# Optimization experiments

Hardware: AMD Instinct MI355X
Metric: run time of the kernel (lower is better)

Reference implementation:

```python
import jax, jax.numpy as jnp
import numpy as np

B, T, D, H = 4096, 256, 64, 96
NEG_SLOPE = 0.01


def setup_inputs() -> dict:
    key = jax.random.key(0)
    ks = jax.random.split(key, 13)
    def n(k, shape, s=0.1):
        return jax.random.normal(k, shape, jnp.float32) * s
    return {
        "x": jax.random.normal(ks[0], (B, T, D), jnp.float32),
        # layer 0 LSTM (PyTorch gate order i,f,g,o); b = b_ih + b_hh fused
        "Wih0": n(ks[1], (4 * H, D)), "Whh0": n(ks[2], (4 * H, H)), "b0": n(ks[3], (4 * H,)),
        # layer 1 LSTM
        "Wih1": n(ks[4], (4 * H, H)), "Whh1": n(ks[5], (4 * H, H)), "b1": n(ks[6], (4 * H,)),
        # MLP head
        "fcW1": n(ks[7], (H, H)), "fcb1": n(ks[8], (H,)),
        "fcW2": n(ks[9], (H, H)), "fcb2": n(ks[10], (H,)),
        "fcW3": n(ks[11], (1, H)), "fcb3": n(ks[12], (1,)),
    }


def _cell(x_t, h, c, Wih, Whh, b):
    # gates: [B, 4H], PyTorch order i, f, g, o
    g = x_t @ Wih.T + h @ Whh.T + b
    i, f, gg, o = jnp.split(g, 4, axis=-1)
    i = jax.nn.sigmoid(i)
    f = jax.nn.sigmoid(f)
    gg = jnp.tanh(gg)
    o = jax.nn.sigmoid(o)
    c_new = f * c + i * gg
    h_new = o * jnp.tanh(c_new)
    return h_new, c_new


def reference(x, Wih0, Whh0, b0, Wih1, Whh1, b1, fcW1, fcb1, fcW2, fcb2, fcW3, fcb3):
    Bx = x.shape[0]
    Hx = Whh0.shape[1]
    xT = jnp.swapaxes(x, 0, 1)  # [T, B, D]
    init = tuple(jnp.zeros((Bx, Hx), x.dtype) for _ in range(4))

    def step(carry, xt):
        h1, c1, h2, c2 = carry
        h1, c1 = _cell(xt, h1, c1, Wih0, Whh0, b0)
        h2, c2 = _cell(h1, h2, c2, Wih1, Whh1, b1)
        return (h1, c1, h2, c2), None

    (h1, c1, h2, c2), _ = jax.lax.scan(step, init, xT)
    last = h2  # out[:, -1, :] == final hidden state of layer 2
    z = jax.nn.leaky_relu(last @ fcW1.T + fcb1, NEG_SLOPE)
    z = jax.nn.leaky_relu(z @ fcW2.T + fcb2, NEG_SLOPE)
    return (z @ fcW3.T + fcb3).squeeze(-1)  # [B]
```

## Files before the change

### kernel.cpp

```cpp
#include <hip/hip_runtime.h>
#include <hip/hip_bf16.h>

#define TT 256
#define NB 16
#define NTHR 768

typedef float f32x4 __attribute__((ext_vector_type(4)));
typedef _Float16 f16x8 __attribute__((ext_vector_type(8)));
typedef __fp16 fp16x2 __attribute__((ext_vector_type(2)));

#define XPAN  0
#define H1PAN 4096
#define H2PAN 12288
#define H2F32 20480
#define FCZ   26624
#define LDSZ  38912

__device__ __forceinline__ float vexp2(float x) { float r; asm("v_exp_f32 %0, %1" : "=v"(r) : "v"(x)); return r; }
__device__ __forceinline__ float vrcp(float x)  { float r; asm("v_rcp_f32 %0, %1" : "=v"(r) : "v"(x)); return r; }
#define L2E 1.44269504f

#define MFMA16(a, b, c) __builtin_amdgcn_mfma_f32_16x16x32_f16(a, b, c, 0, 0, 0)

__device__ __forceinline__ unsigned short f2h_bits(float f) {
    union { _Float16 h; unsigned short u; } cv; cv.h = (_Float16)f; return cv.u;
}

union PK8 { f16x8 v8; fp16x2 v2[4]; };
__device__ __forceinline__ f16x8 pack8(const f32x4& a, const f32x4& b) {
    PK8 U;
    U.v2[0] = __builtin_amdgcn_cvt_pkrtz(a[0], a[1]);
    U.v2[1] = __builtin_amdgcn_cvt_pkrtz(a[2], a[3]);
    U.v2[2] = __builtin_amdgcn_cvt_pkrtz(b[0], b[1]);
    U.v2[3] = __builtin_amdgcn_cvt_pkrtz(b[2], b[3]);
    return U.v8;
}

__global__ void prep_frags16(const float* __restrict__ Wih0, const float* __restrict__ Whh0,
                             const float* __restrict__ Wih1, const float* __restrict__ Whh1,
                             unsigned short* __restrict__ wsf2) {
    int s = blockIdx.x;
    int e = threadIdx.x;
    int i = e & 7, col = (e >> 3) & 15, kg = e >> 7;
    float wv;
    if (s < 48) {
        int ks = s / 24, nt = s % 24;
        int k = ks * 32 + kg * 8 + i, cg = nt * 16 + col;
        wv = Wih0[cg * 64 + k];
    } else if (s < 120) {
        int j = (s - 48) / 24, nt = (s - 48) % 24;
        int k = j * 32 + kg * 8 + i, cg = nt * 16 + col;
        wv = Whh0[cg * 96 + k];
    } else {
        int s2 = s - 120;
        int j = s2 / 24, nt = s2 % 24;
        int k = j * 32 + kg * 8 + i, cg = nt * 16 + col;
        wv = (k < 96) ? Wih1[cg * 96 + k] : Whh1[cg * 96 + (k - 96)];
    }
    wsf2[s * 512 + e] = f2h_bits(wv);
}

__global__ __launch_bounds__(NTHR, 3) void lstm_main(
    const float* __restrict__ x,
    const float* __restrict__ b0, const float* __restrict__ b1,
    const float* __restrict__ fcW1, const float* __restrict__ fcb1,
    const float* __restrict__ fcW2, const float* __restrict__ fcb2,
    const float* __restrict__ fcW3, const float* __restrict__ fcb3,
    const unsigned short* __restrict__ wsf2,
    float* __restrict__ out)
{
    __shared__ __align__(16) char LDS[LDSZ];

    const int tid = threadIdx.x;
    const int lane = tid & 63;
    const int w = tid >> 6;
    const int isB = (w ^ (w >> 2)) & 1;
    const int ub = w >> 1;
    const int l15 = lane & 15, kg = lane >> 4, r7 = l15 & 7;
    const int blk = blockIdx.x;
    const float* xblk = x + (size_t)blk * NB * TT * 64;

    #pragma unroll 1
    for (int i = tid; i < 4096; i += NTHR) ((int*)(LDS + H1PAN))[i] = 0;

    const int cb = ub * 2 + (l15 >> 3);
    const int lo2 = (l15 & 7) * 2;

    const bool stg = (w < 4) && (lane < 32);
    const int st = w * 32 + lane;
    const int sr = st >> 3, su = st & 7;
    const float* xsrc = xblk + (size_t)sr * TT * 64 + su * 8;
    const int xoff = sr * 128 + ((su ^ (sr & 7)) << 4);
    f32x4 xa, xb;

    if (stg) {
        xa = *(const f32x4*)xsrc; xb = *(const f32x4*)(xsrc + 4);
        *(f16x8*)(LDS + XPAN + xoff) = pack8(xa, xb);
    }

    if (!isB) {
        f16x8 F0x[4][2], F0h[4][3];
        #pragma unroll
        for (int g = 0; g < 4; ++g) {
            #pragma unroll
            for (int ks = 0; ks < 2; ++ks)
                F0x[g][ks] = *(const f16x8*)(wsf2 + (ks * 24 + g * 6 + ub) * 512 + lane * 8);
            #pragma unroll
            for (int j = 0; j < 3; ++j)
                F0h[g][j] = *(const f16x8*)(wsf2 + (48 + j * 24 + g * 6 + ub) * 512 + lane * 8);
        }
        float bias[4];
        #pragma unroll
        for (int g = 0; g < 4; ++g) bias[g] = b0[g * 96 + ub * 16 + l15];

        f32x4 c1 = {0.f, 0.f, 0.f, 0.f};
        __syncthreads();

        #pragma unroll 1
        for (int s = 0; s <= TT; ++s) {
            if (stg && s + 1 < TT) {
                const float* xp = xsrc + (size_t)(s + 1) * 64;
                xa = *(const f32x4*)xp; xb = *(const f32x4*)(xp + 4);
            }
            if (s < TT) {
                const char* xr  = LDS + XPAN + ((s & 1) << 11);
                const char* h1r = LDS + H1PAN + (((s & 1) ^ 1) << 12);
                f32x4 a[4];
                #pragma unroll
                for (int g = 0; g < 4; ++g) a[g] = (f32x4){bias[g], bias[g], bias[g], bias[g]};
                __builtin_amdgcn_s_setprio(1);
                #pragma unroll
                for (int ks = 0; ks < 2; ++ks) {
                    int off = l15 * 128 + (((ks * 4 + kg) ^ r7) << 4);
                    f16x8 xh = *(const f16x8*)(xr + off);
                    #pragma unroll
                    for (int g = 0; g < 4; ++g) a[g] = MFMA16(xh, F0x[g][ks], a[g]);
                }
                #pragma unroll
                for (int j = 0; j < 3; ++j) {
                    int off = l15 * 256 + (((j * 4 + kg) ^ r7) << 4);
                    f16x8 ah = *(const f16x8*)(h1r + off);
                    #pragma unroll
                    for (int g = 0; g < 4; ++g) a[g] = MFMA16(ah, F0h[g][j], a[g]);
                }
                __builtin_amdgcn_s_setprio(0);
                char* h1w = LDS + H1PAN + ((s & 1) << 12);
                #pragma unroll
                for (int q = 0; q < 4; ++q) {
                    float ei = vexp2(a[0][q] * (-L2E));
                    float ef = vexp2(a[1][q] * (-L2E));
                    float eg = vexp2(a[2][q] * (-2.f * L2E));
                    float eo = vexp2(a[3][q] * (-L2E));
                    float ivgv = (1.f - eg) * vrcp((1.f + ei) * (1.f + eg));
                    float fv = vrcp(1.f + ef);
                    float cn = fmaf(fv, c1[q], ivgv);
                    c1[q] = cn;
                    float ec = vexp2(cn * (-2.f * L2E));
                    float h = (1.f - ec) * vrcp((1.f + eo) * (1.f + ec));
                    int r_ = kg * 4 + q;
                    int off = r_ * 256 + ((cb ^ (r_ & 7)) << 4) + lo2;
                    *(unsigned short*)(h1w + off) = f2h_bits(h);
                }
            }
            if (stg && s + 1 < TT)
                *(f16x8*)(LDS + XPAN + (((s + 1) & 1) << 11) + xoff) = pack8(xa, xb);
            __syncthreads();
        }
    } else {
        f16x8 F1[4][6];
        #pragma unroll
        for (int g = 0; g < 4; ++g)
            #pragma unroll
            for (int j = 0; j < 6; ++j)
                F1[g][j] = *(const f16x8*)(wsf2 + (120 + j * 24 + g * 6 + ub) * 512 + lane * 8);
        float bias[4];
        #pragma unroll
        for (int g = 0; g < 4; ++g) bias[g] = b1[g * 96 + ub * 16 + l15];

        f32x4 c2 = {0.f, 0.f, 0.f, 0.f};
        __syncthreads();

        #pragma unroll 1
        for (int s = 0; s <= TT; ++s) {
            if (stg && s + 1 < TT) {
                const float* xp = xsrc + (size_t)(s + 1) * 64;
                xa = *(const f32x4*)xp; xb = *(const f32x4*)(xp + 4);
            }
            if (s >= 1) {
                const char* h1r = LDS + H1PAN + (((s & 1) ^ 1) << 12);
                const char* h2r = LDS + H2PAN + ((s & 1) << 12);
                f32x4 a[4];
                #pragma unroll
                for (int g = 0; g < 4; ++g) a[g] = (f32x4){bias[g], bias[g], bias[g], bias[g]};
                __builtin_amdgcn_s_setprio(1);
                #pragma unroll
                for (int j = 0; j < 6; ++j) {
                    const char* pan = (j < 3) ? h1r : h2r;
                    int cc = (j < 3) ? j : j - 3;
                    int off = l15 * 256 + (((cc * 4 + kg) ^ r7) << 4);
                    f16x8 ah = *(const f16x8*)(pan + off);
                    #pragma unroll
                    for (int g = 0; g < 4; ++g) a[g] = MFMA16(ah, F1[g][j], a[g]);
                }
                __builtin_amdgcn_s_setprio(0);
                char* h2w = LDS + H2PAN + ((~s & 1) << 12);
                #pragma unroll
                for (int q = 0; q < 4; ++q) {
                    float ei = vexp2(a[0][q] * (-L2E));
                    float ef = vexp2(a[1][q] * (-L2E));
                    float eg = vexp2(a[2][q] * (-2.f * L2E));
                    float eo = vexp2(a[3][q] * (-L2E));
                    float ivgv = (1.f - eg) * vrcp((1.f + ei) * (1.f + eg));
                    float fv = vrcp(1.f + ef);
                    float cn = fmaf(fv, c2[q], ivgv);
                    c2[q] = cn;
                    float ec = vexp2(cn * (-2.f * L2E));
                    float h = (1.f - ec) * vrcp((1.f + eo) * (1.f + ec));
                    int r_ = kg * 4 + q;
                    int off = r_ * 256 + ((cb ^ (r_ & 7)) << 4) + lo2;
                    *(unsigned short*)(h2w + off) = f2h_bits(h);
                    if (s == TT)
                        ((float*)(LDS + H2F32))[(ub * 16 + l15) * 16 + r_] = h;
                }
            }
            if (stg && s + 1 < TT)
                *(f16x8*)(LDS + XPAN + (((s + 1) & 1) << 11) + xoff) = pack8(xa, xb);
            __syncthreads();
        }
    }
    __syncthreads();

    const float* h2f = (const float*)(LDS + H2F32);
    float* z1 = (float*)(LDS + FCZ);
    float* z2 = z1 + 1536;
    if (tid < 192) {
        int u = tid % 96, half = tid / 96;
        float s0 = fcb1[u];
        for (int r = half * 8; r < half * 8 + 8; ++r) {
            float s = s0;
            #pragma unroll 4
            for (int k = 0; k < 96; ++k) s += fcW1[u * 96 + k] * h2f[k * 16 + r];
            z1[r * 96 + u] = s > 0.f ? s : 0.01f * s;
        }
    }
    __syncthreads();
    if (tid < 192) {
        int u = tid % 96, half = tid / 96;
        float s0 = fcb2[u];
        for (int r = half * 8; r < half * 8 + 8; ++r) {
            float s = s0;
            #pragma unroll 4
            for (int k = 0; k < 96; ++k) s += fcW2[u * 96 + k] * z1[r * 96 + k];
            z2[r * 96 + u] = s > 0.f ? s : 0.01f * s;
        }
    }
    __syncthreads();
    if (tid < NB) {
        float s = fcb3[0];
        #pragma unroll 4
        for (int k = 0; k < 96; ++k) s += fcW3[k] * z2[tid * 96 + k];
        out[blk * NB + tid] = s;
    }
}

extern "C" void kernel_launch(void* const* d_in, const int* in_sizes, int n_in,
                              void* d_out, int out_size, void* d_ws, size_t ws_size,
                              hipStream_t stream) {
    const float* x    = (const float*)d_in[0];
    const float* Wih0 = (const float*)d_in[1];
    const float* Whh0 = (const float*)d_in[2];
    const float* b0   = (const float*)d_in[3];
    const float* Wih1 = (const float*)d_in[4];
    const float* Whh1 = (const float*)d_in[5];
    const float* b1   = (const float*)d_in[6];
    const float* fcW1 = (const float*)d_in[7];
    const float* fcb1 = (const float*)d_in[8];
    const float* fcW2 = (const float*)d_in[9];
    const float* fcb2 = (const float*)d_in[10];
    const float* fcW3 = (const float*)d_in[11];
    const float* fcb3 = (const float*)d_in[12];

    unsigned short* wsf2 = (unsigned short*)d_ws;

    prep_frags16<<<264, 512, 0, stream>>>(Wih0, Whh0, Wih1, Whh1, wsf2);
    lstm_main<<<256, NTHR, 0, stream>>>(x, b0, b1, fcW1, fcb1, fcW2, fcb2,
                                        fcW3, fcb3, wsf2, (float*)d_out);
}
```

Baseline: 406.5 us.

## Replace per-step block barriers with LDS counter-based producer/consumer pipeline

Drops the per-timestep __syncthreads shared by both LSTM layers. Layer-0 and layer-1 wave groups now coordinate through workgroup-scope atomic counters in LDS, using 4-deep ring buffers for the h1 and h2 panels, so the two layers can drift up to a few steps apart. X staging moves onto layer-0 waves only, and the loop drops the extra skew iteration. The aim is to remove lockstep barrier stalls and let layer 0 run ahead, at the cost of spin-wait polling with s_sleep, more LDS, and subtler memory-ordering correctness.

```diff
diff --git a/kernel.cpp b/kernel.cpp
--- a/kernel.cpp
+++ b/kernel.cpp
@@ -11,10 +11,11 @@
 
 #define XPAN  0
 #define H1PAN 4096
-#define H2PAN 12288
-#define H2F32 20480
-#define FCZ   26624
-#define LDSZ  38912
+#define H2PAN 20480
+#define H2F32 36864
+#define FCZ   43008
+#define CNT   55296
+#define LDSZ  55360
 
 __device__ __forceinline__ float vexp2(float x) { float r; asm("v_exp_f32 %0, %1" : "=v"(r) : "v"(x)); return r; }
 __device__ __forceinline__ float vrcp(float x)  { float r; asm("v_rcp_f32 %0, %1" : "=v"(r) : "v"(x)); return r; }
@@ -34,6 +35,19 @@
     U.v2[2] = __builtin_amdgcn_cvt_pkrtz(b[0], b[1]);
     U.v2[3] = __builtin_amdgcn_cvt_pkrtz(b[2], b[3]);
     return U.v8;
+}
+
+__device__ __forceinline__ void spinge(int* cnt, int target) {
+    if (target > 0) {
+        while (__hip_atomic_load(cnt, __ATOMIC_RELAXED, __HIP_MEMORY_SCOPE_WORKGROUP) < target)
+            __builtin_amdgcn_s_sleep(1);
+        __threadfence_block();
+    }
+}
+__device__ __forceinline__ void signal(int* cnt, int lane) {
+    __threadfence_block();
+    if (lane == 0)
+        __hip_atomic_fetch_add(cnt, 1, __ATOMIC_RELAXED, __HIP_MEMORY_SCOPE_WORKGROUP);
 }
 
 __global__ void prep_frags16(const float* __restrict__ Wih0, const float* __restrict__ Whh0,
@@ -80,14 +94,20 @@
     const int blk = blockIdx.x;
     const float* xblk = x + (size_t)blk * NB * TT * 64;
 
+    int* prodH1 = (int*)(LDS + CNT);
+    int* consH1 = (int*)(LDS + CNT) + 1;
+    int* prodH2 = (int*)(LDS + CNT) + 2;
+
     #pragma unroll 1
-    for (int i = tid; i < 4096; i += NTHR) ((int*)(LDS + H1PAN))[i] = 0;
+    for (int i = tid; i < 8192; i += NTHR) ((int*)(LDS + H1PAN))[i] = 0;
+    if (tid < 16) ((int*)(LDS + CNT))[tid] = 0;
 
     const int cb = ub * 2 + (l15 >> 3);
     const int lo2 = (l15 & 7) * 2;
 
-    const bool stg = (w < 4) && (lane < 32);
-    const int st = w * 32 + lane;
+    const int sidx = (w == 0) ? 0 : (w == 2) ? 1 : (w == 5) ? 2 : 3;
+    const bool stg = (w == 0 || w == 2 || w == 5 || w == 7) && (lane < 32);
+    const int st = sidx * 32 + lane;
     const int sr = st >> 3, su = st & 7;
     const float* xsrc = xblk + (size_t)sr * TT * 64 + su * 8;
     const int xoff = sr * 128 + ((su ^ (sr & 7)) << 4);
@@ -97,6 +117,7 @@
         xa = *(const f32x4*)xsrc; xb = *(const f32x4*)(xsrc + 4);
         *(f16x8*)(LDS + XPAN + xoff) = pack8(xa, xb);
     }
+    __syncthreads();
 
     if (!isB) {
         f16x8 F0x[4][2], F0h[4][3];
@@ -114,57 +135,56 @@
         for (int g = 0; g < 4; ++g) bias[g] = b0[g * 96 + ub * 16 + l15];
 
         f32x4 c1 = {0.f, 0.f, 0.f, 0.f};
-        __syncthreads();
 
         #pragma unroll 1
-        for (int s = 0; s <= TT; ++s) {
+        for (int s = 0; s < TT; ++s) {
             if (stg && s + 1 < TT) {
                 const float* xp = xsrc + (size_t)(s + 1) * 64;
                 xa = *(const f32x4*)xp; xb = *(const f32x4*)(xp + 4);
             }
-            if (s < TT) {
-                const char* xr  = LDS + XPAN + ((s & 1) << 11);
-                const char* h1r = LDS + H1PAN + (((s & 1) ^ 1) << 12);
-                f32x4 a[4];
+            spinge(prodH1, 6 * s);
+            const char* xr  = LDS + XPAN + ((s & 1) << 11);
+            const char* h1r = LDS + H1PAN + (((s - 1) & 3) << 12);
+            f32x4 a[4];
+            #pragma unroll
+            for (int g = 0; g < 4; ++g) a[g] = (f32x4){bias[g], bias[g], bias[g], bias[g]};
+            __builtin_amdgcn_s_setprio(1);
+            #pragma unroll
+            for (int ks = 0; ks < 2; ++ks) {
+                int off = l15 * 128 + (((ks * 4 + kg) ^ r7) << 4);
+                f16x8 xh = *(const f16x8*)(xr + off);
                 #pragma unroll
-                for (int g = 0; g < 4; ++g) a[g] = (f32x4){bias[g], bias[g], bias[g], bias[g]};
-                __builtin_amdgcn_s_setprio(1);
+                for (int g = 0; g < 4; ++g) a[g] = MFMA16(xh, F0x[g][ks], a[g]);
+            }
+            #pragma unroll
+            for (int j = 0; j < 3; ++j) {
+                int off = l15 * 256 + (((j * 4 + kg) ^ r7) << 4);
+                f16x8 ah = *(const f16x8*)(h1r + off);
                 #pragma unroll
-                for (int ks = 0; ks < 2; ++ks) {
-                    int off = l15 * 128 + (((ks * 4 + kg) ^ r7) << 4);
-                    f16x8 xh = *(const f16x8*)(xr + off);
-                    #pragma unroll
-                    for (int g = 0; g < 4; ++g) a[g] = MFMA16(xh, F0x[g][ks], a[g]);
-                }
-                #pragma unroll
-                for (int j = 0; j < 3; ++j) {
-                    int off = l15 * 256 + (((j * 4 + kg) ^ r7) << 4);
-                    f16x8 ah = *(const f16x8*)(h1r + off);
-                    #pragma unroll
-                    for (int g = 0; g < 4; ++g) a[g] = MFMA16(ah, F0h[g][j], a[g]);
-                }
-                __builtin_amdgcn_s_setprio(0);
-                char* h1w = LDS + H1PAN + ((s & 1) << 12);
-                #pragma unroll
-                for (int q = 0; q < 4; ++q) {
-                    float ei = vexp2(a[0][q] * (-L2E));
-                    float ef = vexp2(a[1][q] * (-L2E));
-                    float eg = vexp2(a[2][q] * (-2.f * L2E));
-                    float eo = vexp2(a[3][q] * (-L2E));
-                    float ivgv = (1.f - eg) * vrcp((1.f + ei) * (1.f + eg));
-                    float fv = vrcp(1.f + ef);
-                    float cn = fmaf(fv, c1[q], ivgv);
-                    c1[q] = cn;
-                    float ec = vexp2(cn * (-2.f * L2E));
-                    float h = (1.f - ec) * vrcp((1.f + eo) * (1.f + ec));
-                    int r_ = kg * 4 + q;
-                    int off = r_ * 256 + ((cb ^ (r_ & 7)) << 4) + lo2;
-                    *(unsigned short*)(h1w + off) = f2h_bits(h);
-                }
+                for (int g = 0; g < 4; ++g) a[g] = MFMA16(ah, F0h[g][j], a[g]);
+            }
+            __builtin_amdgcn_s_setprio(0);
+            spinge(consH1, 6 * (s - 3));
+            char* h1w = LDS + H1PAN + ((s & 3) << 12);
+            #pragma unroll
+            for (int q = 0; q < 4; ++q) {
+                float ei = vexp2(a[0][q] * (-L2E));
+                float ef = vexp2(a[1][q] * (-L2E));
+                float eg = vexp2(a[2][q] * (-2.f * L2E));
+                float eo = vexp2(a[3][q] * (-L2E));
+                float ivgv = (1.f - eg) * vrcp((1.f + ei) * (1.f + eg));
+                float fv = vrcp(1.f + ef);
+                float cn = fmaf(fv, c1[q], ivgv);
+                c1[q] = cn;
+                float ec = vexp2(cn * (-2.f * L2E));
+                float h = (1.f - ec) * vrcp((1.f + eo) * (1.f + ec));
+                int r_ = kg * 4 + q;
+                int off = r_ * 256 + ((cb ^ (r_ & 7)) << 4) + lo2;
+                *(unsigned short*)(h1w + off) = f2h_bits(h);
             }
             if (stg && s + 1 < TT)
                 *(f16x8*)(LDS + XPAN + (((s + 1) & 1) << 11) + xoff) = pack8(xa, xb);
-            __syncthreads();
+            signal(prodH1, lane);
         }
     } else {
         f16x8 F1[4][6];
@@ -178,54 +198,48 @@
         for (int g = 0; g < 4; ++g) bias[g] = b1[g * 96 + ub * 16 + l15];
 
         f32x4 c2 = {0.f, 0.f, 0.f, 0.f};
-        __syncthreads();
 
         #pragma unroll 1
-        for (int s = 0; s <= TT; ++s) {
-            if (stg && s + 1 < TT) {
-                const float* xp = xsrc + (size_t)(s + 1) * 64;
-                xa = *(const f32x4*)xp; xb = *(const f32x4*)(xp + 4);
-            }
-            if (s >= 1) {
-                const char* h1r = LDS + H1PAN + (((s & 1) ^ 1) << 12);
-                const char* h2r = LDS + H2PAN + ((s & 1) << 12);
-                f32x4 a[4];
+        for (int sp = 0; sp < TT; ++sp) {
+            spinge(prodH1, 6 * (sp + 1));
+            spinge(prodH2, 6 * sp);
+            const char* h1r = LDS + H1PAN + ((sp & 3) << 12);
+            const char* h2r = LDS + H2PAN + (((sp - 1) & 3) << 12);
+            f32x4 a[4];
+            #pragma unroll
+            for (int g = 0; g < 4; ++g) a[g] = (f32x4){bias[g], bias[g], bias[g], bias[g]};
+            __builtin_amdgcn_s_setprio(1);
+            #pragma unroll
+            for (int j = 0; j < 6; ++j) {
+                const char* pan = (j < 3) ? h1r : h2r;
+                int cc = (j < 3) ? j : j - 3;
+                int off = l15 * 256 + (((cc * 4 + kg) ^ r7) << 4);
+                f16x8 ah = *(const f16x8*)(pan + off);
                 #pragma unroll
-                for (int g = 0; g < 4; ++g) a[g] = (f32x4){bias[g], bias[g], bias[g], bias[g]};
-                __builtin_amdgcn_s_setprio(1);
-                #pragma unroll
-                for (int j = 0; j < 6; ++j) {
-                    const char* pan = (j < 3) ? h1r : h2r;
-                    int cc = (j < 3) ? j : j - 3;
-                    int off = l15 * 256 + (((cc * 4 + kg) ^ r7) << 4);
-                    f16x8 ah = *(const f16x8*)(pan + off);
-                    #pragma unroll
-                    for (int g = 0; g < 4; ++g) a[g] = MFMA16(ah, F1[g][j], a[g]);
-                }
-                __builtin_amdgcn_s_setprio(0);
-                char* h2w = LDS + H2PAN + ((~s & 1) << 12);
-                #pragma unroll
-                for (int q = 0; q < 4; ++q) {
-                    float ei = vexp2(a[0][q] * (-L2E));
-                    float ef = vexp2(a[1][q] * (-L2E));
-                    float eg = vexp2(a[2][q] * (-2.f * L2E));
-                    float eo = vexp2(a[3][q] * (-L2E));
-                    float ivgv = (1.f - eg) * vrcp((1.f + ei) * (1.f + eg));
-                    float fv = vrcp(1.f + ef);
-                    float cn = fmaf(fv, c2[q], ivgv);
-                    c2[q] = cn;
-                    float ec = vexp2(cn * (-2.f * L2E));
-                    float h = (1.f - ec) * vrcp((1.f + eo) * (1.f + ec));
-                    int r_ = kg * 4 + q;
-                    int off = r_ * 256 + ((cb ^ (r_ & 7)) << 4) + lo2;
-                    *(unsigned short*)(h2w + off) = f2h_bits(h);
-                    if (s == TT)
-                        ((float*)(LDS + H2F32))[(ub * 16 + l15) * 16 + r_] = h;
-                }
-            }
-            if (stg && s + 1 < TT)
-                *(f16x8*)(LDS + XPAN + (((s + 1) & 1) << 11) + xoff) = pack8(xa, xb);
-            __syncthreads();
+                for (int g = 0; g < 4; ++g) a[g] = MFMA16(ah, F1[g][j], a[g]);
+            }
+            __builtin_amdgcn_s_setprio(0);
+            signal(consH1, lane);
+            char* h2w = LDS + H2PAN + ((sp & 3) << 12);
+            #pragma unroll
+            for (int q = 0; q < 4; ++q) {
+                float ei = vexp2(a[0][q] * (-L2E));
+                float ef = vexp2(a[1][q] * (-L2E));
+                float eg = vexp2(a[2][q] * (-2.f * L2E));
+                float eo = vexp2(a[3][q] * (-L2E));
+                float ivgv = (1.f - eg) * vrcp((1.f + ei) * (1.f + eg));
+                float fv = vrcp(1.f + ef);
+                float cn = fmaf(fv, c2[q], ivgv);
+                c2[q] = cn;
+                float ec = vexp2(cn * (-2.f * L2E));
+                float h = (1.f - ec) * vrcp((1.f + eo) * (1.f + ec));
+                int r_ = kg * 4 + q;
+                int off = r_ * 256 + ((cb ^ (r_ & 7)) << 4) + lo2;
+                *(unsigned short*)(h2w + off) = f2h_bits(h);
+                if (sp == TT - 1)
+                    ((float*)(LDS + H2F32))[(ub * 16 + l15) * 16 + r_] = h;
+            }
+            signal(prodH2, lane);
         }
     }
     __syncthreads();
```

Result: faster. 395.7 us (-2.7%).
